# Kernel optimization log

Measured on AMD Instinct MI355X. Metric: run time of the kernel, lower is better.

## Reference

```python
import jax, jax.numpy as jnp
import numpy as np

B, S, D = 8, 1024, 128
EPS = 1e-7
LN_EPS = 1e-3  # keras LayerNormalization default


def setup_inputs() -> dict:
    key = jax.random.key(0)
    ks = jax.random.split(key, 8)
    sd = 1.0 / np.sqrt(D)
    return {
        "x": jax.random.normal(ks[0], (B, S, D), jnp.float32),
        "Wq": jax.random.normal(ks[1], (D, D), jnp.float32) * sd,
        "bq": jnp.zeros((D,), jnp.float32),
        "Wm": jax.random.normal(ks[2], (D, D), jnp.float32) * sd,
        "bm": jnp.zeros((D,), jnp.float32),
        "Ww": jax.random.normal(ks[3], (D, 1), jnp.float32) * sd,
        "bw": jnp.zeros((1,), jnp.float32),
        "Wc": jax.random.normal(ks[4], (D, 1), jnp.float32) * sd,
        "bc": jnp.zeros((1,), jnp.float32),
        "emb_map": jax.random.normal(ks[5], (D, D, D), jnp.float32) * 0.02,
        "gamma": jnp.ones((D,), jnp.float32),
        "beta": jnp.zeros((D,), jnp.float32),
    }


def reference(x, Wq, bq, Wm, bm, Ww, bw, Wc, bc, emb_map, gamma, beta):
    b_, s_, d_ = x.shape
    q = x @ Wq + bq                      # [B,S,D]
    m = jax.nn.sigmoid(x @ Wm + bm)      # [B,S,D]
    w = jax.nn.relu(x @ Ww + bw)         # [B,S,1]
    c = jax.nn.relu(x @ Wc + bc)         # [B,S,1]

    # distances: for query pos i, preceding pos j (j<i) has distance i-j
    idx = jnp.arange(s_)
    dist = (idx[:, None] - idx[None, :]).astype(x.dtype)   # [S,S]
    valid = dist > 0                                       # strict causal
    # cosh positional decay, zero outside causal window -> [B,S,S]
    pe = jnp.where(valid[None], 1.0 / jnp.cosh((dist[None] - c) / (w + EPS)), 0.0)

    # angle between (pe * x_j * m_i + eps) and (q_i + eps), expanded analytically
    qp = q + EPS
    t1 = jnp.einsum('bjd,bid->bij', x, m * qp)             # sum_d x_j m_i q'_i
    s1 = jnp.einsum('bjd,bid->bij', x, m)                  # sum_d x_j m_i
    s2 = jnp.einsum('bjd,bid->bij', x * x, m * m)          # sum_d (x_j m_i)^2
    dot = pe * t1 + EPS * jnp.sum(qp, axis=-1)[:, :, None]
    na = jnp.sqrt(pe * pe * s2 + 2.0 * EPS * pe * s1 + d_ * EPS * EPS)
    nb = jnp.linalg.norm(qp, axis=-1)[:, :, None]
    cos = jnp.where(valid[None], dot / (na * nb), 0.0)
    angle = jnp.where(valid[None], jnp.arccos(cos), 0.0)   # [B,S,S]

    # query_result_i = sum_j pe*angle * x_j  -> [B,S,D]
    qr = jnp.einsum('bij,bjd->bid', pe * angle, x)

    # embedding matrix: current_token (rows) outer query_result (cols),
    # contracted against rank-3 map: out[b,s,d] = sum_{j,k} x[b,s,j] qr[b,s,k] map[d,j,k]
    em = jnp.einsum('bsj,bsk->bsjk', x, qr).reshape(b_, s_, d_ * d_)
    mapped = em @ emb_map.reshape(d_, d_ * d_).T           # [B,S,D]

    res = mapped + x
    mu = jnp.mean(res, axis=-1, keepdims=True)
    var = jnp.var(res, axis=-1, keepdims=True)
    out = (res - mu) / jnp.sqrt(var + LN_EPS) * gamma + beta
    return out  # dropout is identity at inference
```

## Files before the change

### kernel.cpp

```cpp
#include <hip/hip_runtime.h>
#include <hip/hip_bf16.h>
#include <math.h>

#define DD 128
#define SS 1024
#define NROWS 8192
#define EPSF 1e-7f
#define LN_EPSF 1e-3f
#define TCUT 30.0f

typedef __attribute__((ext_vector_type(8))) short bf16x8;
typedef __attribute__((ext_vector_type(4))) float f32x4;
typedef __attribute__((ext_vector_type(16))) float f32x16;

__device__ __forceinline__ void gload_lds16(const void* g, void* l) {
    __builtin_amdgcn_global_load_lds(
        (const __attribute__((address_space(1))) unsigned int*)g,
        (__attribute__((address_space(3))) unsigned int*)l, 16, 0, 0);
}
__device__ __forceinline__ short f2bf(float v) {
    union { __hip_bfloat16 h; short s; } u;
    u.h = __float2bfloat16(v);
    return u.s;
}
__device__ __forceinline__ float bf2f(short s) {
    union { __hip_bfloat16 h; short s; } u; u.s = s;
    return __bfloat162float(u.h);
}

__global__ __launch_bounds__(256) void k0a_emb(const float* __restrict__ emb,
                                               short* __restrict__ embh3) {
    __shared__ float lt[32][128];
    int d = blockIdx.x, js = blockIdx.y, t = threadIdx.x;
    {
        int jl = t >> 3, k0 = (t & 7) * 16;
        const float4* src = (const float4*)(emb + (size_t)d * 16384
                                            + (size_t)(js * 32 + jl) * 128 + k0);
#pragma unroll
        for (int q = 0; q < 4; ++q) *(float4*)&lt[jl][k0 + q * 4] = src[q];
    }
    __syncthreads();
    int ks = t >> 5, l0 = (t & 31) * 2;
    union { bf16x8 v[2]; short s[16]; } ob;
#pragma unroll
    for (int li = 0; li < 2; ++li) {
        int l = l0 + li;
        const float* p = &lt[l & 31][ks * 16 + (l >> 5) * 8];
#pragma unroll
        for (int e = 0; e < 8; ++e) ob.s[li * 8 + e] = f2bf(p[e]);
    }
    short* dst = embh3 + (size_t)(d * 4 + js) * 4096 + (size_t)t * 16;
    *(bf16x8*)dst = ob.v[0];
    *(bf16x8*)(dst + 8) = ob.v[1];
}

__global__ __launch_bounds__(256) void k0w_split(const float* __restrict__ Wq,
        const float* __restrict__ Wm, short* __restrict__ Wfrag) {
    int T = blockIdx.x * 256 + threadIdx.x;
    int e = T & 7, l = (T >> 3) & 63, ks = (T >> 9) & 3, nt = (T >> 11) & 7,
        mat = (T >> 14) & 1;
    int k = ks * 32 + ((l >> 4) & 3) * 8 + e;
    int c = nt * 16 + (l & 15);
    float v = (mat ? Wm : Wq)[k * 128 + c];
    short h = f2bf(v);
    float lo = v - bf2f(h);
    Wfrag[((((size_t)(mat * 2 + 0) * 8 + nt) * 4 + ks) * 64 + l) * 8 + e] = h;
    Wfrag[((((size_t)(mat * 2 + 1) * 8 + nt) * 4 + ks) * 64 + l) * 8 + e] = f2bf(lo);
}

__global__ __launch_bounds__(256) void k0c_xsplit(const float* __restrict__ x,
        const float* __restrict__ Ww, const float* __restrict__ bw,
        const float* __restrict__ Wc, const float* __restrict__ bc,
        short* __restrict__ xh2, short* __restrict__ xl2,
        float* __restrict__ scal) {
    __shared__ float xs[32][129];
    int rb = blockIdx.x, t = threadIdx.x;
    {
        int r = t >> 3, d0 = (t & 7) * 16;
        const float4* src = (const float4*)(x + (size_t)(rb * 32 + r) * 128 + d0);
#pragma unroll
        for (int q = 0; q < 4; ++q) *(float4*)&xs[r][d0 + q * 4] = src[q];
    }
    __syncthreads();
    int ks = (t >> 5) & 3, rf = t >> 7, l0 = (t & 31) * 2;
    union { bf16x8 v[2]; short s[16]; } hb, lb;
#pragma unroll
    for (int li = 0; li < 2; ++li) {
        int l = l0 + li;
        const float* p = &xs[rf * 16 + (l & 15)][ks * 32 + ((l >> 4) & 3) * 8];
#pragma unroll
        for (int e = 0; e < 8; ++e) {
            float v = p[e];
            short h = f2bf(v);
            hb.s[li * 8 + e] = h;
            lb.s[li * 8 + e] = f2bf(v - bf2f(h));
        }
    }
    {
        short* d1 = xh2 + (size_t)rb * 4096 + (size_t)t * 16;
        short* d2 = xl2 + (size_t)rb * 4096 + (size_t)t * 16;
        *(bf16x8*)d1 = hb.v[0]; *(bf16x8*)(d1 + 8) = hb.v[1];
        *(bf16x8*)d2 = lb.v[0]; *(bf16x8*)(d2 + 8) = lb.v[1];
    }
    int rr = t >> 3, seg = t & 7;
    float pw = 0.f, pc = 0.f;
#pragma unroll
    for (int dq = 0; dq < 16; ++dq) {
        float xv = xs[rr][seg * 16 + dq];
        pw = fmaf(xv, Ww[seg * 16 + dq], pw);
        pc = fmaf(xv, Wc[seg * 16 + dq], pc);
    }
    pw += __shfl_xor(pw, 1); pw += __shfl_xor(pw, 2); pw += __shfl_xor(pw, 4);
    pc += __shfl_xor(pc, 1); pc += __shfl_xor(pc, 2); pc += __shfl_xor(pc, 4);
    if (seg == 0) {
        scal[(size_t)(rb * 32 + rr) * 4 + 0] = fmaxf(pw + bw[0], 0.f);
        scal[(size_t)(rb * 32 + rr) * 4 + 1] = fmaxf(pc + bc[0], 0.f);
    }
}

__global__ __launch_bounds__(256) void k1_mfma(
    const short* __restrict__ xh2, const short* __restrict__ xl2,
    const short* __restrict__ Wfrag,
    const float* __restrict__ bq, const float* __restrict__ bm,
    float* __restrict__ mq, float* __restrict__ mo, float* __restrict__ scal)
{
    __shared__ __align__(16) short wl[65536];
    __shared__ float red[32][4][2];
    int t = threadIdx.x, w = t >> 6, l = t & 63;
    int l15 = l & 15, g = l >> 4;
    int row0 = blockIdx.x * 32;
#pragma unroll
    for (int it = 0; it < 32; ++it)
        gload_lds16(Wfrag + (size_t)(it * 256 + t) * 8, wl + (size_t)(it * 256 + w * 64) * 8);
    const short* xb  = xh2 + (size_t)blockIdx.x * 4096;
    const short* xlb = xl2 + (size_t)blockIdx.x * 4096;
    bf16x8 Ah[2][4], Al[2][4];
#pragma unroll
    for (int rf = 0; rf < 2; ++rf)
#pragma unroll
        for (int ks = 0; ks < 4; ++ks) {
            size_t o = ((size_t)(rf * 4 + ks) * 64 + l) * 8;
            Ah[rf][ks] = *(const bf16x8*)(xb + o);
            Al[rf][ks] = *(const bf16x8*)(xlb + o);
        }
    __syncthreads();
    f32x4 accq[2][2] = {}, accm[2][2] = {};
#pragma unroll
    for (int ntp = 0; ntp < 2; ++ntp) {
        int nt = w * 2 + ntp;
#pragma unroll
        for (int ks = 0; ks < 4; ++ks) {
            bf16x8 bhq = *(const bf16x8*)(wl + ((size_t)(0  + nt) * 4 + ks) * 512 + l * 8);
            bf16x8 blq = *(const bf16x8*)(wl + ((size_t)(8  + nt) * 4 + ks) * 512 + l * 8);
            bf16x8 bhm = *(const bf16x8*)(wl + ((size_t)(16 + nt) * 4 + ks) * 512 + l * 8);
            bf16x8 blm = *(const bf16x8*)(wl + ((size_t)(24 + nt) * 4 + ks) * 512 + l * 8);
#pragma unroll
            for (int rf = 0; rf < 2; ++rf) {
                accq[rf][ntp] = __builtin_amdgcn_mfma_f32_16x16x32_bf16(Ah[rf][ks], bhq, accq[rf][ntp], 0, 0, 0);
                accq[rf][ntp] = __builtin_amdgcn_mfma_f32_16x16x32_bf16(Ah[rf][ks], blq, accq[rf][ntp], 0, 0, 0);
                accq[rf][ntp] = __builtin_amdgcn_mfma_f32_16x16x32_bf16(Al[rf][ks], bhq, accq[rf][ntp], 0, 0, 0);
                accm[rf][ntp] = __builtin_amdgcn_mfma_f32_16x16x32_bf16(Ah[rf][ks], bhm, accm[rf][ntp], 0, 0, 0);
                accm[rf][ntp] = __builtin_amdgcn_mfma_f32_16x16x32_bf16(Ah[rf][ks], blm, accm[rf][ntp], 0, 0, 0);
                accm[rf][ntp] = __builtin_amdgcn_mfma_f32_16x16x32_bf16(Al[rf][ks], bhm, accm[rf][ntp], 0, 0, 0);
            }
        }
    }
    float sq1[2][4] = {{0,0,0,0},{0,0,0,0}};
    float sq2[2][4] = {{0,0,0,0},{0,0,0,0}};
#pragma unroll
    for (int ntp = 0; ntp < 2; ++ntp) {
        int c = (w * 2 + ntp) * 16 + l15;
        float bqv = bq[c] + EPSF, bmv = bm[c];
#pragma unroll
        for (int rf = 0; rf < 2; ++rf)
#pragma unroll
            for (int reg = 0; reg < 4; ++reg) {
                int rloc = rf * 16 + g * 4 + reg;
                float qp = accq[rf][ntp][reg] + bqv;
                float mv = 1.0f / (1.0f + expf(-(accm[rf][ntp][reg] + bmv)));
                size_t o = (size_t)(row0 + rloc) * 128 + c;
                mq[o] = mv * qp;
                mo[o] = mv;
                sq1[rf][reg] += qp;
                sq2[rf][reg] += qp * qp;
            }
    }
#pragma unroll
    for (int rf = 0; rf < 2; ++rf)
#pragma unroll
        for (int reg = 0; reg < 4; ++reg) {
            float a = sq1[rf][reg], b = sq2[rf][reg];
            a += __shfl_xor(a, 1); a += __shfl_xor(a, 2);
            a += __shfl_xor(a, 4); a += __shfl_xor(a, 8);
            b += __shfl_xor(b, 1); b += __shfl_xor(b, 2);
            b += __shfl_xor(b, 4); b += __shfl_xor(b, 8);
            if (l15 == 0) {
                red[rf * 16 + g * 4 + reg][w][0] = a;
                red[rf * 16 + g * 4 + reg][w][1] = b;
            }
        }
    __syncthreads();
    if (t < 32) {
        float a = red[t][0][0] + red[t][1][0] + red[t][2][0] + red[t][3][0];
        float b = red[t][0][1] + red[t][1][1] + red[t][2][1] + red[t][3][1];
        scal[(size_t)(row0 + t) * 4 + 2] = a;
        scal[(size_t)(row0 + t) * 4 + 3] = sqrtf(b);
    }
}

__global__ __launch_bounds__(256) void k2_qr(
    const float* __restrict__ x,
    const float* __restrict__ mq, const float* __restrict__ mo,
    const float* __restrict__ scal, short* __restrict__ qrh2)
{
    int row = blockIdx.x;
    int i = row & (SS - 1);
    const float* xb = x + (size_t)(row - i) * DD;
    int t = threadIdx.x, w = t >> 6, l = t & 63;
    int sub = l >> 4, q = l & 15;
    int qo = q * 8;

    float mqv[8], mov[8];
    {
        const float* mp = mq + (size_t)row * DD + qo;
        float4 a = *(const float4*)mp, b = *(const float4*)(mp + 4);
        mqv[0] = a.x; mqv[1] = a.y; mqv[2] = a.z; mqv[3] = a.w;
        mqv[4] = b.x; mqv[5] = b.y; mqv[6] = b.z; mqv[7] = b.w;
        const float* op = mo + (size_t)row * DD + qo;
        float4 c = *(const float4*)op, d = *(const float4*)(op + 4);
        mov[0] = c.x; mov[1] = c.y; mov[2] = c.z; mov[3] = c.w;
        mov[4] = d.x; mov[5] = d.y; mov[6] = d.z; mov[7] = d.w;
    }
    float wv = scal[row * 4 + 0], cv = scal[row * 4 + 1];
    float sumqp = scal[row * 4 + 2], nb = scal[row * 4 + 3];
    float wi = wv + EPSF;
    float dmaxf = cv + TCUT * wi;
    int dmax = (dmaxf >= (float)i) ? i : (int)dmaxf;

    float acc[8] = {0.f, 0.f, 0.f, 0.f, 0.f, 0.f, 0.f, 0.f};
    int nit = (dmax + 15) >> 4;
    int dbase = 1 + w * 4 + sub;
    for (int it = 0; it < nit; ++it) {
        int dist = dbase + it * 16;
        float xv[8];
        if (dist <= dmax) {
            const float* xp = xb + (size_t)(i - dist) * DD + qo;
            float4 a = *(const float4*)xp, b = *(const float4*)(xp + 4);
            xv[0] = a.x; xv[1] = a.y; xv[2] = a.z; xv[3] = a.w;
            xv[4] = b.x; xv[5] = b.y; xv[6] = b.z; xv[7] = b.w;
        } else {
#pragma unroll
            for (int e = 0; e < 8; ++e) xv[e] = 0.f;
        }
        float t1 = 0.f, s1 = 0.f, s2 = 0.f;
#pragma unroll
        for (int e = 0; e < 8; ++e) {
            float xm = xv[e] * mov[e];
            t1 = fmaf(xv[e], mqv[e], t1);
            s1 += xm;
            s2 = fmaf(xm, xm, s2);
        }
#pragma unroll
        for (int off = 1; off < 16; off <<= 1) {
            t1 += __shfl_xor(t1, off);
            s1 += __shfl_xor(s1, off);
            s2 += __shfl_xor(s2, off);
        }
        float tt = ((float)dist - cv) / wi;
        float pe = 1.0f / coshf(tt);
        float dotv = fmaf(pe, t1, EPSF * sumqp);
        float na = sqrtf(fmaf(pe * pe, s2,
                         fmaf(2.0f * EPSF * pe, s1, (float)DD * EPSF * EPSF)));
        float cosv = fminf(1.0f, fmaxf(-1.0f, dotv / (na * nb)));
        float ang = acosf(cosv);
        float wgt = pe * ang;
#pragma unroll
        for (int e = 0; e < 8; ++e) acc[e] = fmaf(wgt, xv[e], acc[e]);
    }
#pragma unroll
    for (int e = 0; e < 8; ++e) {
        acc[e] += __shfl_xor(acc[e], 16);
        acc[e] += __shfl_xor(acc[e], 32);
    }
    __shared__ float sq[4][DD];
    if (l < 16) {
#pragma unroll
        for (int e = 0; e < 8; ++e) sq[w][qo + e] = acc[e];
    }
    __syncthreads();
    if (t < DD) {
        float v = sq[0][t] + sq[1][t] + sq[2][t] + sq[3][t];
        int rbq = row >> 7, rr = row & 127, rt2 = rr >> 5, lp = rr & 31;
        int k = t;
        qrh2[(((size_t)(rbq * 4 + rt2) * 8 + (k >> 4)) * 64
              + (lp + 32 * ((k >> 3) & 1))) * 8 + (k & 7)] = f2bf(v);
    }
}

__global__ __launch_bounds__(256, 1) void k3_gemm(
    const float* __restrict__ x, const short* __restrict__ embh3,
    const short* __restrict__ qrh2, float* __restrict__ part)
{
    __shared__ float xt[32][128];
    __shared__ __align__(16) float sbuf[4][128][36];
    int t = threadIdx.x, w = t >> 6, l = t & 63;
    int l31 = l & 31, hi = l >> 5;
    int rb = blockIdx.x, js = blockIdx.y;
    {
        int rr = t >> 3, j4 = (t & 7) * 4;
#pragma unroll
        for (int it = 0; it < 4; ++it) {
            int r = it * 32 + rr;
            float4 v = *(const float4*)(x + (size_t)(rb * 128 + r) * 128 + js * 32 + j4);
            xt[j4][r] = v.x; xt[j4 + 1][r] = v.y; xt[j4 + 2][r] = v.z; xt[j4 + 3][r] = v.w;
        }
    }
    bf16x8 Bf[4][8];
    const short* qb = qrh2 + (size_t)rb * 16384;
#pragma unroll
    for (int rt = 0; rt < 4; ++rt)
#pragma unroll
        for (int ks = 0; ks < 8; ++ks)
            Bf[rt][ks] = *(const bf16x8*)(qb + (size_t)((rt * 8 + ks) * 64 + l) * 8);
    __syncthreads();
    float xv[4][16];
#pragma unroll
    for (int rt = 0; rt < 4; ++rt)
#pragma unroll
        for (int reg = 0; reg < 16; ++reg) {
            int rowj = (reg & 3) + 8 * (reg >> 2) + 4 * hi;
            xv[rt][reg] = xt[rowj][rt * 32 + l31];
        }
    float (*sw)[36] = sbuf[w];
    const short* Ab = embh3 + (size_t)(w * 128 + js) * 4096;
    bf16x8 A0[8], A1[8];
#pragma unroll
    for (int ks = 0; ks < 8; ++ks)
        A0[ks] = *(const bf16x8*)(Ab + (size_t)ks * 512 + l * 8);

#define K3_COMPUTE(AF, COL)                                                     \
    {                                                                           \
        f32x16 acc[4];                                                          \
        _Pragma("unroll")                                                       \
        for (int rt = 0; rt < 4; ++rt)                                          \
            _Pragma("unroll")                                                   \
            for (int q = 0; q < 16; ++q) acc[rt][q] = 0.f;                      \
        _Pragma("unroll")                                                       \
        for (int ks = 0; ks < 8; ++ks)                                          \
            _Pragma("unroll")                                                   \
            for (int rt = 0; rt < 4; ++rt)                                      \
                acc[rt] = __builtin_amdgcn_mfma_f32_32x32x16_bf16(              \
                    AF[ks], Bf[rt][ks], acc[rt], 0, 0, 0);                      \
        _Pragma("unroll")                                                       \
        for (int rt = 0; rt < 4; ++rt) {                                        \
            float s = 0.f;                                                      \
            _Pragma("unroll")                                                   \
            for (int reg = 0; reg < 16; ++reg)                                  \
                s = fmaf(xv[rt][reg], acc[rt][reg], s);                         \
            s += __shfl_xor(s, 32);                                             \
            if (l < 32) sw[rt * 32 + l][COL] = s;                               \
        }                                                                       \
    }

#pragma unroll 1
    for (int i = 0; i < 32; i += 2) {
        const short* An = Ab + (size_t)(i + 1) * 16384;
#pragma unroll
        for (int ks = 0; ks < 8; ++ks)
            A1[ks] = *(const bf16x8*)(An + (size_t)ks * 512 + l * 8);
        K3_COMPUTE(A0, i)
        if (i + 2 < 32) {
            const short* An2 = Ab + (size_t)(i + 2) * 16384;
#pragma unroll
            for (int ks = 0; ks < 8; ++ks)
                A0[ks] = *(const bf16x8*)(An2 + (size_t)ks * 512 + l * 8);
        }
        K3_COMPUTE(A1, i + 1)
    }
#undef K3_COMPUTE
#pragma unroll
    for (int ii = 0; ii < 16; ++ii) {
        int r = ii * 8 + (l >> 3);
        int dl = (l & 7) * 4;
        float4 v = *(const float4*)&sw[r][dl];
        *(float4*)(part + (size_t)js * (NROWS * DD)
                   + (size_t)(rb * 128 + r) * 128 + w * 32 + dl) = v;
    }
}

__global__ __launch_bounds__(256) void k4_ln(
    const float* __restrict__ x, const float* __restrict__ part,
    const float* __restrict__ gamma, const float* __restrict__ beta,
    float* __restrict__ out)
{
    int wave = threadIdx.x >> 6, lane = threadIdx.x & 63;
    int row = blockIdx.x * 4 + wave;
    size_t base = (size_t)row * DD;
    float r0 = x[base + lane], r1 = x[base + lane + 64];
#pragma unroll
    for (int p = 0; p < 4; ++p) {
        r0 += part[(size_t)p * NROWS * DD + base + lane];
        r1 += part[(size_t)p * NROWS * DD + base + lane + 64];
    }
    float s = r0 + r1, s2 = r0 * r0 + r1 * r1;
#pragma unroll
    for (int off = 32; off > 0; off >>= 1) {
        s += __shfl_xor(s, off);
        s2 += __shfl_xor(s2, off);
    }
    float mu = s * (1.0f / DD);
    float var = s2 * (1.0f / DD) - mu * mu;
    var = fmaxf(var, 0.0f);
    float rs = rsqrtf(var + LN_EPSF);
    out[base + lane] = (r0 - mu) * rs * gamma[lane] + beta[lane];
    out[base + lane + 64] = (r1 - mu) * rs * gamma[lane + 64] + beta[lane + 64];
}

extern "C" void kernel_launch(void* const* d_in, const int* in_sizes, int n_in,
                              void* d_out, int out_size, void* d_ws, size_t ws_size,
                              hipStream_t stream) {
    const float* x     = (const float*)d_in[0];
    const float* Wq    = (const float*)d_in[1];
    const float* bq    = (const float*)d_in[2];
    const float* Wm    = (const float*)d_in[3];
    const float* bm    = (const float*)d_in[4];
    const float* Ww    = (const float*)d_in[5];
    const float* bw    = (const float*)d_in[6];
    const float* Wc    = (const float*)d_in[7];
    const float* bc    = (const float*)d_in[8];
    const float* emb   = (const float*)d_in[9];
    const float* gamma = (const float*)d_in[10];
    const float* beta  = (const float*)d_in[11];
    float* out = (float*)d_out;
    float* ws  = (float*)d_ws;

    short* embh3 = (short*)ws;
    short* qrh2  = (short*)(ws + 1048576);
    float* scal  = ws + 1572864;
    float* part  = ws + 1605632;
    short* xh2   = (short*)part;
    short* xl2   = (short*)(part + 524288);
    float* mq    = part + 1048576;
    float* mo    = part + 2097152;
    short* Wfrag = (short*)(part + 3145728);

    hipLaunchKernelGGL(k0a_emb,   dim3(128, 4), dim3(256), 0, stream, emb, embh3);
    hipLaunchKernelGGL(k0w_split, dim3(256),    dim3(256), 0, stream, Wq, Wm, Wfrag);
    hipLaunchKernelGGL(k0c_xsplit,dim3(256),    dim3(256), 0, stream,
                       x, Ww, bw, Wc, bc, xh2, xl2, scal);
    hipLaunchKernelGGL(k1_mfma,   dim3(256),    dim3(256), 0, stream,
                       xh2, xl2, Wfrag, bq, bm, mq, mo, scal);
    hipLaunchKernelGGL(k2_qr,     dim3(8192),   dim3(256), 0, stream,
                       x, mq, mo, scal, qrh2);
    hipLaunchKernelGGL(k3_gemm,   dim3(64, 4),  dim3(256), 0, stream,
                       x, embh3, qrh2, part);
    hipLaunchKernelGGL(k4_ln,     dim3(2048),   dim3(256), 0, stream,
                       x, part, gamma, beta, out);
}
```

Baseline: 92.38 us.

## Repartition k3_gemm across 8 waves splitting row tiles and output halves

The k3 embedding GEMM now launches 512 threads per block instead of 256. Each wave owns one 32-row tile and half of the output dimension, rather than every wave covering all four row tiles for a quarter of the outputs. This shrinks per-wave B-fragment and accumulator register use, and the A loads are double-buffered two at a time. Partial sums go to one shared 128x129 buffer that is written out after a block barrier. The intent is more waves in flight to hide the emb_map loads, at the cost of each wave re-reading A fragments across row tiles.

```diff
diff --git a/kernel.cpp b/kernel.cpp
--- a/kernel.cpp
+++ b/kernel.cpp
@@ -297,94 +297,105 @@
     }
 }
 
-__global__ __launch_bounds__(256, 1) void k3_gemm(
+__global__ __launch_bounds__(512, 2) void k3_gemm(
     const float* __restrict__ x, const short* __restrict__ embh3,
     const short* __restrict__ qrh2, float* __restrict__ part)
 {
-    __shared__ float xt[32][128];
-    __shared__ __align__(16) float sbuf[4][128][36];
-    int t = threadIdx.x, w = t >> 6, l = t & 63;
+    __shared__ float xt[32][132];
+    __shared__ __align__(16) float sbuf[128][129];
+    int t = threadIdx.x, w8 = t >> 6, l = t & 63;
     int l31 = l & 31, hi = l >> 5;
+    int rt = w8 & 3, dh = w8 >> 2;
     int rb = blockIdx.x, js = blockIdx.y;
+
     {
-        int rr = t >> 3, j4 = (t & 7) * 4;
-#pragma unroll
-        for (int it = 0; it < 4; ++it) {
-            int r = it * 32 + rr;
-            float4 v = *(const float4*)(x + (size_t)(rb * 128 + r) * 128 + js * 32 + j4);
-            xt[j4][r] = v.x; xt[j4 + 1][r] = v.y; xt[j4 + 2][r] = v.z; xt[j4 + 3][r] = v.w;
-        }
-    }
-    bf16x8 Bf[4][8];
+        int r = t & 127, jq = (t >> 7) * 8;
+        const float* xp = x + (size_t)(rb * 128 + r) * 128 + js * 32 + jq;
+        float4 a = *(const float4*)xp, b = *(const float4*)(xp + 4);
+        xt[jq + 0][r] = a.x; xt[jq + 1][r] = a.y;
+        xt[jq + 2][r] = a.z; xt[jq + 3][r] = a.w;
+        xt[jq + 4][r] = b.x; xt[jq + 5][r] = b.y;
+        xt[jq + 6][r] = b.z; xt[jq + 7][r] = b.w;
+    }
+
+    bf16x8 Bf[8];
     const short* qb = qrh2 + (size_t)rb * 16384;
 #pragma unroll
-    for (int rt = 0; rt < 4; ++rt)
-#pragma unroll
-        for (int ks = 0; ks < 8; ++ks)
-            Bf[rt][ks] = *(const bf16x8*)(qb + (size_t)((rt * 8 + ks) * 64 + l) * 8);
-    __syncthreads();
-    float xv[4][16];
-#pragma unroll
-    for (int rt = 0; rt < 4; ++rt)
-#pragma unroll
-        for (int reg = 0; reg < 16; ++reg) {
-            int rowj = (reg & 3) + 8 * (reg >> 2) + 4 * hi;
-            xv[rt][reg] = xt[rowj][rt * 32 + l31];
-        }
-    float (*sw)[36] = sbuf[w];
-    const short* Ab = embh3 + (size_t)(w * 128 + js) * 4096;
-    bf16x8 A0[8], A1[8];
-#pragma unroll
     for (int ks = 0; ks < 8; ++ks)
-        A0[ks] = *(const bf16x8*)(Ab + (size_t)ks * 512 + l * 8);
-
-#define K3_COMPUTE(AF, COL)                                                     \
-    {                                                                           \
-        f32x16 acc[4];                                                          \
-        _Pragma("unroll")                                                       \
-        for (int rt = 0; rt < 4; ++rt)                                          \
-            _Pragma("unroll")                                                   \
-            for (int q = 0; q < 16; ++q) acc[rt][q] = 0.f;                      \
-        _Pragma("unroll")                                                       \
-        for (int ks = 0; ks < 8; ++ks)                                          \
-            _Pragma("unroll")                                                   \
-            for (int rt = 0; rt < 4; ++rt)                                      \
-                acc[rt] = __builtin_amdgcn_mfma_f32_32x32x16_bf16(              \
-                    AF[ks], Bf[rt][ks], acc[rt], 0, 0, 0);                      \
-        _Pragma("unroll")                                                       \
-        for (int rt = 0; rt < 4; ++rt) {                                        \
-            float s = 0.f;                                                      \
-            _Pragma("unroll")                                                   \
-            for (int reg = 0; reg < 16; ++reg)                                  \
-                s = fmaf(xv[rt][reg], acc[rt][reg], s);                         \
-            s += __shfl_xor(s, 32);                                             \
-            if (l < 32) sw[rt * 32 + l][COL] = s;                               \
-        }                                                                       \
+        Bf[ks] = *(const bf16x8*)(qb + (size_t)((rt * 8 + ks) * 64 + l) * 8);
+
+    __syncthreads();
+    float xv[16];
+#pragma unroll
+    for (int reg = 0; reg < 16; ++reg) {
+        int rowj = (reg & 3) + 8 * (reg >> 2) + 4 * hi;
+        xv[reg] = xt[rowj][rt * 32 + l31];
+    }
+
+    const short* Abp = embh3 + (size_t)(dh * 256 + js) * 4096 + (size_t)l * 8;
+
+    bf16x8 Aa[8], Ab2[8], Ac[8], Ad2[8];
+#pragma unroll
+    for (int ks = 0; ks < 8; ++ks) {
+        Aa[ks]  = *(const bf16x8*)(Abp + (size_t)ks * 512);
+        Ab2[ks] = *(const bf16x8*)(Abp + 16384 + (size_t)ks * 512);
+    }
+
+#define COMP(AR, DI)                                                        \
+    {                                                                       \
+        f32x16 acc;                                                         \
+        _Pragma("unroll")                                                   \
+        for (int q = 0; q < 16; ++q) acc[q] = 0.f;                          \
+        _Pragma("unroll")                                                   \
+        for (int ks = 0; ks < 8; ++ks)                                      \
+            acc = __builtin_amdgcn_mfma_f32_32x32x16_bf16(AR[ks], Bf[ks],   \
+                                                          acc, 0, 0, 0);    \
+        float s0 = 0.f, s1 = 0.f, s2 = 0.f, s3 = 0.f;                       \
+        _Pragma("unroll")                                                   \
+        for (int q = 0; q < 4; ++q) {                                       \
+            s0 = fmaf(xv[q * 4 + 0], acc[q * 4 + 0], s0);                   \
+            s1 = fmaf(xv[q * 4 + 1], acc[q * 4 + 1], s1);                   \
+            s2 = fmaf(xv[q * 4 + 2], acc[q * 4 + 2], s2);                   \
+            s3 = fmaf(xv[q * 4 + 3], acc[q * 4 + 3], s3);                   \
+        }                                                                   \
+        float s = (s0 + s1) + (s2 + s3);                                    \
+        s += __shfl_xor(s, 32);                                             \
+        if (hi == 0) sbuf[rt * 32 + l31][DI] = s;                           \
     }
 
 #pragma unroll 1
-    for (int i = 0; i < 32; i += 2) {
-        const short* An = Ab + (size_t)(i + 1) * 16384;
-#pragma unroll
-        for (int ks = 0; ks < 8; ++ks)
-            A1[ks] = *(const bf16x8*)(An + (size_t)ks * 512 + l * 8);
-        K3_COMPUTE(A0, i)
-        if (i + 2 < 32) {
-            const short* An2 = Ab + (size_t)(i + 2) * 16384;
-#pragma unroll
-            for (int ks = 0; ks < 8; ++ks)
-                A0[ks] = *(const bf16x8*)(An2 + (size_t)ks * 512 + l * 8);
-        }
-        K3_COMPUTE(A1, i + 1)
-    }
-#undef K3_COMPUTE
-#pragma unroll
-    for (int ii = 0; ii < 16; ++ii) {
-        int r = ii * 8 + (l >> 3);
-        int dl = (l & 7) * 4;
-        float4 v = *(const float4*)&sw[r][dl];
+    for (int i = 0; i < 64; i += 4) {
+        {
+            const short* An = Abp + (size_t)(i + 2) * 16384;
+#pragma unroll
+            for (int ks = 0; ks < 8; ++ks) {
+                Ac[ks]  = *(const bf16x8*)(An + (size_t)ks * 512);
+                Ad2[ks] = *(const bf16x8*)(An + 16384 + (size_t)ks * 512);
+            }
+        }
+        COMP(Aa,  dh * 64 + i)
+        COMP(Ab2, dh * 64 + i + 1)
+        if (i + 4 < 64) {
+            const short* An = Abp + (size_t)(i + 4) * 16384;
+#pragma unroll
+            for (int ks = 0; ks < 8; ++ks) {
+                Aa[ks]  = *(const bf16x8*)(An + (size_t)ks * 512);
+                Ab2[ks] = *(const bf16x8*)(An + 16384 + (size_t)ks * 512);
+            }
+        }
+        COMP(Ac,  dh * 64 + i + 2)
+        COMP(Ad2, dh * 64 + i + 3)
+    }
+#undef COMP
+
+    __syncthreads();
+#pragma unroll
+    for (int e = 0; e < 8; ++e) {
+        int idx4 = e * 512 + t;
+        int r = idx4 >> 5, c4 = (idx4 & 31) * 4;
         *(float4*)(part + (size_t)js * (NROWS * DD)
-                   + (size_t)(rb * 128 + r) * 128 + w * 32 + dl) = v;
+                   + (size_t)(rb * 128 + r) * 128 + c4)
+            = *(const float4*)&sbuf[r][c4];
     }
 }
 
@@ -452,7 +463,7 @@
                        xh2, xl2, Wfrag, bq, bm, mq, mo, scal);
     hipLaunchKernelGGL(k2_qr,     dim3(8192),   dim3(256), 0, stream,
                        x, mq, mo, scal, qrh2);
-    hipLaunchKernelGGL(k3_gemm,   dim3(64, 4),  dim3(256), 0, stream,
+    hipLaunchKernelGGL(k3_gemm,   dim3(64, 4),  dim3(512), 0, stream,
                        x, embh3, qrh2, part);
     hipLaunchKernelGGL(k4_ln,     dim3(2048),   dim3(256), 0, stream,
                        x, part, gamma, beta, out);
```

Result: slower. 96.45 us (+4.4%).

## Retile embedding-map GEMM over row chunks, output slices and K halves with bf16 partials

Applied to the files above, without the earlier changes.

The k3 embedding GEMM is restructured onto a 3D grid (row chunk, output-d group, j-slice) with 512-thread blocks. Each block stages its slice of the bf16 emb map into LDS via direct global-to-LDS loads, and waves split the K dimension in halves. x is held in LDS as bf16 and partial outputs are written as bf16, so k4 sums eight bf16 partials instead of four fp32 ones. The aim is more parallelism (1024 blocks instead of 256), more reuse of the emb tiles and less partial-sum traffic, at the cost of extra bf16 rounding in x and in the partial sums.

```diff
diff --git a/kernel.cpp b/kernel.cpp
--- a/kernel.cpp
+++ b/kernel.cpp
@@ -26,6 +26,14 @@
 __device__ __forceinline__ float bf2f(short s) {
     union { __hip_bfloat16 h; short s; } u; u.s = s;
     return __bfloat162float(u.h);
+}
+__device__ __forceinline__ unsigned int pack_bf16(float lo, float hi) {
+    unsigned int r;
+    asm("v_cvt_pk_bf16_f32 %0, %1, %2" : "=v"(r) : "v"(lo), "v"(hi));
+    return r;
+}
+__device__ __forceinline__ float u2f(unsigned int u) {
+    union { unsigned int u; float f; } c; c.u = u; return c.f;
 }
 
 __global__ __launch_bounds__(256) void k0a_emb(const float* __restrict__ emb,
@@ -297,99 +305,128 @@
     }
 }
 
-__global__ __launch_bounds__(256, 1) void k3_gemm(
+__global__ __launch_bounds__(512, 2) void k3_gemm(
     const float* __restrict__ x, const short* __restrict__ embh3,
-    const short* __restrict__ qrh2, float* __restrict__ part)
+    const short* __restrict__ qrh2, short* __restrict__ partb)
 {
-    __shared__ float xt[32][128];
-    __shared__ __align__(16) float sbuf[4][128][36];
-    int t = threadIdx.x, w = t >> 6, l = t & 63;
+    __shared__ __align__(16) char ldsb[81920];
+    short* xtwh = (short*)ldsb;
+    short* elds = (short*)ldsb;
+    short* swb  = (short*)(ldsb + 65536);
+
+    int t = threadIdx.x, w8 = t >> 6, l = t & 63;
     int l31 = l & 31, hi = l >> 5;
-    int rb = blockIdx.x, js = blockIdx.y;
-    {
-        int rr = t >> 3, j4 = (t & 7) * 4;
-#pragma unroll
-        for (int it = 0; it < 4; ++it) {
-            int r = it * 32 + rr;
-            float4 v = *(const float4*)(x + (size_t)(rb * 128 + r) * 128 + js * 32 + j4);
-            xt[j4][r] = v.x; xt[j4 + 1][r] = v.y; xt[j4 + 2][r] = v.z; xt[j4 + 3][r] = v.w;
-        }
-    }
-    bf16x8 Bf[4][8];
-    const short* qb = qrh2 + (size_t)rb * 16384;
+    int kp = w8 & 1, rh = w8 >> 1;
+    int rc = blockIdx.x, dq = blockIdx.y, js = blockIdx.z;
+
+#pragma unroll
+    for (int i = 0; i < 8; ++i) {
+        int idx = i * 512 + t;
+        int r = idx >> 3, j4 = (idx & 7) * 4;
+        float4 v = *(const float4*)(x + (size_t)(rc * 512 + r) * 128 + js * 32 + j4);
+        *(unsigned int*)(xtwh + r * 36 + j4)     = pack_bf16(v.x, v.y);
+        *(unsigned int*)(xtwh + r * 36 + j4 + 2) = pack_bf16(v.z, v.w);
+    }
+
+    bf16x8 Bf[4][4];
+    int rbq = rc * 4 + rh;
 #pragma unroll
     for (int rt = 0; rt < 4; ++rt)
 #pragma unroll
-        for (int ks = 0; ks < 8; ++ks)
-            Bf[rt][ks] = *(const bf16x8*)(qb + (size_t)((rt * 8 + ks) * 64 + l) * 8);
-    __syncthreads();
+        for (int s = 0; s < 4; ++s)
+            Bf[rt][s] = *(const bf16x8*)(qrh2
+                + (((size_t)(rbq * 4 + rt) * 8 + kp * 4 + s) * 64 + l) * 8);
+
+    __syncthreads();
+
     float xv[4][16];
 #pragma unroll
-    for (int rt = 0; rt < 4; ++rt)
-#pragma unroll
-        for (int reg = 0; reg < 16; ++reg) {
-            int rowj = (reg & 3) + 8 * (reg >> 2) + 4 * hi;
-            xv[rt][reg] = xt[rowj][rt * 32 + l31];
-        }
-    float (*sw)[36] = sbuf[w];
-    const short* Ab = embh3 + (size_t)(w * 128 + js) * 4096;
-    bf16x8 A0[8], A1[8];
-#pragma unroll
-    for (int ks = 0; ks < 8; ++ks)
-        A0[ks] = *(const bf16x8*)(Ab + (size_t)ks * 512 + l * 8);
-
-#define K3_COMPUTE(AF, COL)                                                     \
-    {                                                                           \
-        f32x16 acc[4];                                                          \
-        _Pragma("unroll")                                                       \
-        for (int rt = 0; rt < 4; ++rt)                                          \
-            _Pragma("unroll")                                                   \
-            for (int q = 0; q < 16; ++q) acc[rt][q] = 0.f;                      \
-        _Pragma("unroll")                                                       \
-        for (int ks = 0; ks < 8; ++ks)                                          \
-            _Pragma("unroll")                                                   \
-            for (int rt = 0; rt < 4; ++rt)                                      \
-                acc[rt] = __builtin_amdgcn_mfma_f32_32x32x16_bf16(              \
-                    AF[ks], Bf[rt][ks], acc[rt], 0, 0, 0);                      \
-        _Pragma("unroll")                                                       \
-        for (int rt = 0; rt < 4; ++rt) {                                        \
-            float s = 0.f;                                                      \
-            _Pragma("unroll")                                                   \
-            for (int reg = 0; reg < 16; ++reg)                                  \
-                s = fmaf(xv[rt][reg], acc[rt][reg], s);                         \
-            s += __shfl_xor(s, 32);                                             \
-            if (l < 32) sw[rt * 32 + l][COL] = s;                               \
-        }                                                                       \
-    }
-
-#pragma unroll 1
-    for (int i = 0; i < 32; i += 2) {
-        const short* An = Ab + (size_t)(i + 1) * 16384;
-#pragma unroll
-        for (int ks = 0; ks < 8; ++ks)
-            A1[ks] = *(const bf16x8*)(An + (size_t)ks * 512 + l * 8);
-        K3_COMPUTE(A0, i)
-        if (i + 2 < 32) {
-            const short* An2 = Ab + (size_t)(i + 2) * 16384;
-#pragma unroll
-            for (int ks = 0; ks < 8; ++ks)
-                A0[ks] = *(const bf16x8*)(An2 + (size_t)ks * 512 + l * 8);
-        }
-        K3_COMPUTE(A1, i + 1)
-    }
-#undef K3_COMPUTE
-#pragma unroll
-    for (int ii = 0; ii < 16; ++ii) {
-        int r = ii * 8 + (l >> 3);
-        int dl = (l & 7) * 4;
-        float4 v = *(const float4*)&sw[r][dl];
-        *(float4*)(part + (size_t)js * (NROWS * DD)
-                   + (size_t)(rb * 128 + r) * 128 + w * 32 + dl) = v;
+    for (int rt = 0; rt < 4; ++rt) {
+        int row_l = rh * 128 + rt * 32 + l31;
+#pragma unroll
+        for (int p = 0; p < 8; ++p) {
+            int jA = ((2 * p) & 3) + 8 * (p >> 1) + 4 * hi;
+            unsigned int u = *(const unsigned int*)(xtwh + row_l * 36 + jA);
+            xv[rt][2 * p]     = u2f(u << 16);
+            xv[rt][2 * p + 1] = u2f(u & 0xFFFF0000u);
+        }
+    }
+
+    __syncthreads();
+
+#pragma unroll
+    for (int i = 0; i < 8; ++i) {
+        int c = i * 512 + t;
+        int d = c >> 9, off = c & 511;
+        gload_lds16(embh3 + (size_t)((dq * 8 + d) * 4 + js) * 4096 + (size_t)off * 8,
+                    elds + (size_t)(i * 512 + w8 * 64) * 8);
+    }
+    __syncthreads();
+
+    float sprev[4];
+    short* swbase = swb + (kp * 512 + rh * 128 + l31) * 8;
+
+#define K3_DSTEP(DI, ODD)                                                    \
+    {                                                                        \
+        bf16x8 A[4];                                                         \
+        _Pragma("unroll")                                                    \
+        for (int s = 0; s < 4; ++s)                                          \
+            A[s] = *(const bf16x8*)(elds + (DI) * 4096                       \
+                                    + ((kp * 4 + s) * 64 + l) * 8);          \
+        _Pragma("unroll")                                                    \
+        for (int rtp = 0; rtp < 2; ++rtp) {                                  \
+            f32x16 ac0, ac1;                                                 \
+            _Pragma("unroll")                                                \
+            for (int q = 0; q < 16; ++q) { ac0[q] = 0.f; ac1[q] = 0.f; }     \
+            _Pragma("unroll")                                                \
+            for (int s = 0; s < 4; ++s) {                                    \
+                ac0 = __builtin_amdgcn_mfma_f32_32x32x16_bf16(               \
+                    A[s], Bf[rtp * 2][s], ac0, 0, 0, 0);                     \
+                ac1 = __builtin_amdgcn_mfma_f32_32x32x16_bf16(               \
+                    A[s], Bf[rtp * 2 + 1][s], ac1, 0, 0, 0);                 \
+            }                                                                \
+            float sm0 = 0.f, sm1 = 0.f;                                      \
+            _Pragma("unroll")                                                \
+            for (int q = 0; q < 16; ++q) {                                   \
+                sm0 = fmaf(xv[rtp * 2][q], ac0[q], sm0);                     \
+                sm1 = fmaf(xv[rtp * 2 + 1][q], ac1[q], sm1);                 \
+            }                                                                \
+            sm0 += __shfl_xor(sm0, 32);                                      \
+            sm1 += __shfl_xor(sm1, 32);                                      \
+            if (ODD) {                                                       \
+                if (hi == 0) {                                               \
+                    *(unsigned int*)(swbase + rtp * 2 * 32 * 8 + (DI) - 1)   \
+                        = pack_bf16(sprev[rtp * 2], sm0);                    \
+                    *(unsigned int*)(swbase + (rtp * 2 + 1) * 32 * 8 + (DI) - 1) \
+                        = pack_bf16(sprev[rtp * 2 + 1], sm1);                \
+                }                                                            \
+            } else {                                                         \
+                sprev[rtp * 2] = sm0;                                        \
+                sprev[rtp * 2 + 1] = sm1;                                    \
+            }                                                                \
+        }                                                                    \
+    }
+
+#pragma unroll
+    for (int dp = 0; dp < 4; ++dp) {
+        K3_DSTEP(2 * dp, 0)
+        K3_DSTEP(2 * dp + 1, 1)
+    }
+#undef K3_DSTEP
+
+    __syncthreads();
+#pragma unroll
+    for (int i = 0; i < 2; ++i) {
+        int c = i * 512 + t;
+        int kp2 = c >> 9, rl = c & 511;
+        *(bf16x8*)(partb + (size_t)(js * 2 + kp2) * 1048576
+                   + (size_t)(rc * 512 + rl) * 128 + dq * 8)
+            = *(const bf16x8*)(swb + (kp2 * 512 + rl) * 8);
     }
 }
 
 __global__ __launch_bounds__(256) void k4_ln(
-    const float* __restrict__ x, const float* __restrict__ part,
+    const float* __restrict__ x, const short* __restrict__ partb,
     const float* __restrict__ gamma, const float* __restrict__ beta,
     float* __restrict__ out)
 {
@@ -398,9 +435,9 @@
     size_t base = (size_t)row * DD;
     float r0 = x[base + lane], r1 = x[base + lane + 64];
 #pragma unroll
-    for (int p = 0; p < 4; ++p) {
-        r0 += part[(size_t)p * NROWS * DD + base + lane];
-        r1 += part[(size_t)p * NROWS * DD + base + lane + 64];
+    for (int p = 0; p < 8; ++p) {
+        r0 += bf2f(partb[(size_t)p * 1048576 + base + lane]);
+        r1 += bf2f(partb[(size_t)p * 1048576 + base + lane + 64]);
     }
     float s = r0 + r1, s2 = r0 * r0 + r1 * r1;
 #pragma unroll
@@ -437,12 +474,13 @@
     short* embh3 = (short*)ws;
     short* qrh2  = (short*)(ws + 1048576);
     float* scal  = ws + 1572864;
-    float* part  = ws + 1605632;
-    short* xh2   = (short*)part;
-    short* xl2   = (short*)(part + 524288);
-    float* mq    = part + 1048576;
-    float* mo    = part + 2097152;
-    short* Wfrag = (short*)(part + 3145728);
+    short* partb = (short*)(ws + 1605632);
+    float* tr    = ws + 1605632;
+    short* xh2   = (short*)tr;
+    short* xl2   = (short*)(tr + 524288);
+    float* mq    = tr + 1048576;
+    float* mo    = tr + 2097152;
+    short* Wfrag = (short*)(tr + 3145728);
 
     hipLaunchKernelGGL(k0a_emb,   dim3(128, 4), dim3(256), 0, stream, emb, embh3);
     hipLaunchKernelGGL(k0w_split, dim3(256),    dim3(256), 0, stream, Wq, Wm, Wfrag);
@@ -452,8 +490,8 @@
                        xh2, xl2, Wfrag, bq, bm, mq, mo, scal);
     hipLaunchKernelGGL(k2_qr,     dim3(8192),   dim3(256), 0, stream,
                        x, mq, mo, scal, qrh2);
-    hipLaunchKernelGGL(k3_gemm,   dim3(64, 4),  dim3(256), 0, stream,
-                       x, embh3, qrh2, part);
+    hipLaunchKernelGGL(k3_gemm,   dim3(16, 16, 4), dim3(512), 0, stream,
+                       x, embh3, qrh2, partb);
     hipLaunchKernelGGL(k4_ln,     dim3(2048),   dim3(256), 0, stream,
-                       x, part, gamma, beta, out);
-}
+                       x, partb, gamma, beta, out);
+}
```

New measurement: 92.98 us. No clear change (+0.7%).
